# Performance work log

Measured on AMD Instinct MI355X. Metric: run time of the kernel, lower is better.

## Reference

```python
import jax, jax.numpy as jnp
import numpy as np

N_NODES = 50000
N_EDGES = 800000
IN_DIM = 1280
HID = 512
EMB = 64
LN_EPS = 1e-5
NEG_SLOPE = 0.2  # DGL GATConv default leaky_relu slope


def setup_inputs() -> dict:
    key = jax.random.key(0)
    ks = jax.random.split(key, 10)
    features = jax.random.normal(ks[0], (N_NODES, IN_DIM), dtype=jnp.float32)
    src = jax.random.randint(ks[1], (N_EDGES,), 0, N_NODES)
    dst = jax.random.randint(ks[2], (N_EDGES,), 0, N_NODES)
    # MLPBlock params: Linear(IN_DIM -> HID) + LayerNorm(HID)
    W1 = jax.random.normal(ks[3], (IN_DIM, HID), dtype=jnp.float32) / np.sqrt(IN_DIM)
    b1 = jnp.zeros((HID,), dtype=jnp.float32)
    ln_g = jnp.ones((HID,), dtype=jnp.float32)
    ln_b = jnp.zeros((HID,), dtype=jnp.float32)
    # GATConv params (num_heads=1): fc (no bias), attn_l, attn_r, output bias
    Wg = jax.random.normal(ks[4], (HID, EMB), dtype=jnp.float32) / np.sqrt(HID)
    attn_l = jax.random.normal(ks[5], (EMB,), dtype=jnp.float32) * 0.1
    attn_r = jax.random.normal(ks[6], (EMB,), dtype=jnp.float32) * 0.1
    bias_g = jnp.zeros((EMB,), dtype=jnp.float32)
    return {"features": features, "src": src, "dst": dst, "W1": W1, "b1": b1,
            "ln_g": ln_g, "ln_b": ln_b, "Wg": Wg, "attn_l": attn_l,
            "attn_r": attn_r, "bias_g": bias_g}


def reference(features, src, dst, W1, b1, ln_g, ln_b, Wg, attn_l, attn_r, bias_g):
    # MLPBlock: linear -> ReLU -> LayerNorm (dropout is identity in eval)
    x = jax.nn.relu(features @ W1 + b1)                     # [N, HID]
    mu = jnp.mean(x, axis=-1, keepdims=True)
    var = jnp.mean(jnp.square(x - mu), axis=-1, keepdims=True)
    x = (x - mu) * jax.lax.rsqrt(var + LN_EPS) * ln_g + ln_b

    # GATConv (single head)
    feat = x @ Wg                                           # [N, EMB]
    el = feat @ attn_l                                      # [N]
    er = feat @ attn_r                                      # [N]
    e = jax.nn.leaky_relu(el[src] + er[dst], NEG_SLOPE)     # [E]

    # edge softmax over incoming edges of each dst node
    m = jax.ops.segment_max(e, dst, num_segments=N_NODES)   # [N]
    ex = jnp.exp(e - m[dst])                                # [E]
    s = jax.ops.segment_sum(ex, dst, num_segments=N_NODES)  # [N]
    a = ex / s[dst]                                         # [E]

    # scatter-aggregate weighted source features
    out = jax.ops.segment_sum(a[:, None] * feat[src], dst, num_segments=N_NODES)
    return out + bias_g                                     # [N, EMB] (head dim squeezed)
```

## Files before the change

### kernel.cpp

```cpp
#include <hip/hip_runtime.h>
#include <hip/hip_bf16.h>
#include <stdint.h>

#define N_NODES 50000
#define N_EDGES 800000
#define IN_DIM 1280
#define HID 512
#define EMB 64
#define M_PAD 50048
#define MT1 391
#define LN_EPS 1e-5f

typedef __attribute__((ext_vector_type(8))) __bf16 bf16x8;
typedef __attribute__((ext_vector_type(4))) float floatx4;

#define AS1C(p) ((const __attribute__((address_space(1))) void*)(p))
#define AS3(p)  ((__attribute__((address_space(3))) void*)(p))

__device__ __forceinline__ unsigned f2bf(float f) {
  unsigned u = __float_as_uint(f);
  u += 0x7FFFu + ((u >> 16) & 1u);
  return u >> 16;
}
__device__ __forceinline__ float bf2f(unsigned short s) {
  return __uint_as_float(((unsigned)s) << 16);
}

__global__ __launch_bounds__(256) void k_prep(const float* __restrict__ W1,
                                              const float* __restrict__ Wg,
                                              const float* __restrict__ ln_g,
                                              const float* __restrict__ ln_b,
                                              unsigned short* __restrict__ B1t,
                                              unsigned short* __restrict__ Wgp,
                                              float* __restrict__ uvec,
                                              float* __restrict__ vvec,
                                              int* __restrict__ deg,
                                              float* __restrict__ s1,
                                              float* __restrict__ s2) {
  int idx = blockIdx.x * 256 + threadIdx.x;
  if (idx < HID * IN_DIM) {
    int n = idx / IN_DIM;
    int k = idx - n * IN_DIM;
    B1t[idx] = (unsigned short)f2bf(W1[(size_t)k * HID + n]);
  }
  if (idx < EMB * HID) {
    int n = idx >> 9;
    int k = idx & 511;
    Wgp[idx] = (unsigned short)f2bf(ln_g[k] * Wg[(size_t)k * EMB + n]);
  }
  if (idx < EMB) {
    float su = 0.f, sv = 0.f;
    for (int k = 0; k < HID; ++k) {
      float wv = Wg[(size_t)k * EMB + idx];
      su += ln_b[k] * wv;
      sv += ln_g[k] * wv;
    }
    uvec[idx] = su;
    vvec[idx] = sv;
  }
  if (idx < N_NODES) deg[idx] = 0;
  if (idx < M_PAD) { s1[idx] = 0.f; s2[idx] = 0.f; }
}

__global__ __launch_bounds__(256) void k_convhist(const float* __restrict__ F,
                                                  unsigned short* __restrict__ Fb,
                                                  const int* __restrict__ dst,
                                                  int* __restrict__ deg) {
  if (blockIdx.x < 31280) {
    size_t base = ((size_t)blockIdx.x * 256 + threadIdx.x) * 8;
    uint4 o;
    if (base < (size_t)N_NODES * IN_DIM) {
      float4 f0 = *(const float4*)(F + base);
      float4 f1 = *(const float4*)(F + base + 4);
      o.x = f2bf(f0.x) | (f2bf(f0.y) << 16);
      o.y = f2bf(f0.z) | (f2bf(f0.w) << 16);
      o.z = f2bf(f1.x) | (f2bf(f1.y) << 16);
      o.w = f2bf(f1.z) | (f2bf(f1.w) << 16);
    } else {
      o = make_uint4(0u, 0u, 0u, 0u);
    }
    *(uint4*)(Fb + base) = o;
  } else {
    int t = (blockIdx.x - 31280) * 256 + threadIdx.x;
    if (t < N_EDGES) atomicAdd(&deg[dst[t]], 1);
  }
}

__global__ __launch_bounds__(256) void k_gemm1(const unsigned short* __restrict__ Abf,
                                               const unsigned short* __restrict__ Bt,
                                               const float* __restrict__ bias1,
                                               unsigned short* __restrict__ xn,
                                               float* __restrict__ s1,
                                               float* __restrict__ s2) {
  __shared__ unsigned short As[128 * 64];
  __shared__ unsigned short Bs[128 * 64];
  const int t = threadIdx.x;
  const int bm = blockIdx.x, bn = blockIdx.y;
  const int w = t >> 6, lane = t & 63, quad = lane >> 4, lr = lane & 15;
  const int wm = (w & 1) * 64, wn = (w >> 1) * 64;

  floatx4 acc[4][4];
#pragma unroll
  for (int i = 0; i < 4; ++i)
#pragma unroll
    for (int j = 0; j < 4; ++j) acc[i][j] = (floatx4){0.f, 0.f, 0.f, 0.f};

  const int rr = t >> 3;
  const int cc = (t & 7) ^ (rr & 7);
  const unsigned short* aP[4];
  const unsigned short* bP[4];
#pragma unroll
  for (int j = 0; j < 4; ++j) {
    aP[j] = Abf + (size_t)(bm * 128 + j * 32 + rr) * IN_DIM + cc * 8;
    bP[j] = Bt + (size_t)(bn * 128 + j * 32 + rr) * IN_DIM + cc * 8;
  }
  unsigned short* asw = As + w * 512;
  unsigned short* bsw = Bs + w * 512;

  const int l7 = lr & 7;

  for (int k0 = 0; k0 < IN_DIM; k0 += 64) {
#pragma unroll
    for (int j = 0; j < 4; ++j) {
      __builtin_amdgcn_global_load_lds(AS1C(aP[j] + k0), AS3(asw + j * 2048), 16, 0, 0);
      __builtin_amdgcn_global_load_lds(AS1C(bP[j] + k0), AS3(bsw + j * 2048), 16, 0, 0);
    }
    __syncthreads();

#pragma unroll
    for (int h = 0; h < 2; ++h) {
      const int col = ((h * 4 + quad) ^ l7) * 8;
      bf16x8 af[4], bfv[4];
#pragma unroll
      for (int mi = 0; mi < 4; ++mi)
        af[mi] = *(const bf16x8*)&As[(wm + mi * 16 + lr) * 64 + col];
#pragma unroll
      for (int ni = 0; ni < 4; ++ni)
        bfv[ni] = *(const bf16x8*)&Bs[(wn + ni * 16 + lr) * 64 + col];
#pragma unroll
      for (int mi = 0; mi < 4; ++mi)
#pragma unroll
        for (int ni = 0; ni < 4; ++ni)
          acc[mi][ni] = __builtin_amdgcn_mfma_f32_16x16x32_bf16(af[mi], bfv[ni], acc[mi][ni], 0, 0, 0);
    }
    __syncthreads();
  }

#pragma unroll
  for (int mi = 0; mi < 4; ++mi) {
    int gr = bm * 128 + wm + mi * 16 + quad * 4;
#pragma unroll
    for (int r = 0; r < 4; ++r) {
      float ps1 = 0.f, ps2 = 0.f;
#pragma unroll
      for (int ni = 0; ni < 4; ++ni) {
        int gc = bn * 128 + wn + ni * 16 + lr;
        float v = acc[mi][ni][r] + bias1[gc];
        v = v > 0.f ? v : 0.f;
        unsigned short h = (unsigned short)f2bf(v);
        xn[(size_t)(gr + r) * HID + gc] = h;
        float vr = bf2f(h);
        ps1 += vr;
        ps2 += vr * vr;
      }
#pragma unroll
      for (int m = 1; m < 16; m <<= 1) {
        ps1 += __shfl_xor(ps1, m, 64);
        ps2 += __shfl_xor(ps2, m, 64);
      }
      if (lr == 0) {
        atomicAdd(&s1[gr + r], ps1);
        atomicAdd(&s2[gr + r], ps2);
      }
    }
  }
}

__device__ __forceinline__ int swz(int r) { return (r ^ (r >> 2)) & 3; }

__global__ __launch_bounds__(256) void k_gemm2(const unsigned short* __restrict__ Xn,
                                               const unsigned short* __restrict__ Wgp,
                                               const float* __restrict__ s1,
                                               const float* __restrict__ s2,
                                               const float* __restrict__ uvec,
                                               const float* __restrict__ vvec,
                                               const float* __restrict__ al,
                                               const float* __restrict__ ar,
                                               float* __restrict__ feat,
                                               float* __restrict__ el,
                                               float* __restrict__ er) {
  __shared__ unsigned short As[128 * 32];
  __shared__ unsigned short Bs[64 * 32];
  const int t = threadIdx.x;
  const int bm = blockIdx.x;
  const int w = t >> 6, lane = t & 63, quad = lane >> 4, lr = lane & 15;

  floatx4 acc[2][4];
#pragma unroll
  for (int i = 0; i < 2; ++i)
#pragma unroll
    for (int j = 0; j < 4; ++j) acc[i][j] = (floatx4){0.f, 0.f, 0.f, 0.f};

  const int r0 = t >> 2, c0 = (t & 3) ^ swz(t >> 2);
  const int r1 = 64 + (t >> 2), c1 = (t & 3) ^ swz(64 + (t >> 2));
  const unsigned short* a0 = Xn + (size_t)(bm * 128 + r0) * HID + c0 * 8;
  const unsigned short* a1 = Xn + (size_t)(bm * 128 + r1) * HID + c1 * 8;
  const unsigned short* b0 = Wgp + (size_t)r0 * HID + c0 * 8;
  unsigned short* asw = As + w * 512;
  unsigned short* bsw = Bs + w * 512;

  const int q2 = quad ^ swz(lr);

  for (int k0 = 0; k0 < HID; k0 += 32) {
    __builtin_amdgcn_global_load_lds(AS1C(a0 + k0), AS3(asw), 16, 0, 0);
    __builtin_amdgcn_global_load_lds(AS1C(a1 + k0), AS3(asw + 2048), 16, 0, 0);
    __builtin_amdgcn_global_load_lds(AS1C(b0 + k0), AS3(bsw), 16, 0, 0);
    __syncthreads();

    bf16x8 af[2], bfv[4];
#pragma unroll
    for (int mi = 0; mi < 2; ++mi)
      af[mi] = *(const bf16x8*)&As[(w * 32 + mi * 16 + lr) * 32 + q2 * 8];
#pragma unroll
    for (int ni = 0; ni < 4; ++ni)
      bfv[ni] = *(const bf16x8*)&Bs[(ni * 16 + lr) * 32 + q2 * 8];
#pragma unroll
    for (int mi = 0; mi < 2; ++mi)
#pragma unroll
      for (int ni = 0; ni < 4; ++ni)
        acc[mi][ni] = __builtin_amdgcn_mfma_f32_16x16x32_bf16(af[mi], bfv[ni], acc[mi][ni], 0, 0, 0);
    __syncthreads();
  }

  float alv[4], arv[4], uv[4], vv[4];
#pragma unroll
  for (int ni = 0; ni < 4; ++ni) {
    alv[ni] = al[ni * 16 + lr];
    arv[ni] = ar[ni * 16 + lr];
    uv[ni] = uvec[ni * 16 + lr];
    vv[ni] = vvec[ni * 16 + lr];
  }
#pragma unroll
  for (int mi = 0; mi < 2; ++mi) {
    int gr = bm * 128 + w * 32 + mi * 16 + quad * 4;
#pragma unroll
    for (int r = 0; r < 4; ++r) {
      int row = gr + r;
      float mu = s1[row] * (1.f / HID);
      float rs = rsqrtf(s2[row] * (1.f / HID) - mu * mu + LN_EPS);
      float mrs = mu * rs;
      float sl = 0.f, sr2 = 0.f;
#pragma unroll
      for (int ni = 0; ni < 4; ++ni) {
        float v = rs * acc[mi][ni][r] + uv[ni] - mrs * vv[ni];
        feat[(size_t)row * EMB + ni * 16 + lr] = v;
        sl += v * alv[ni];
        sr2 += v * arv[ni];
      }
#pragma unroll
      for (int m = 1; m < 16; m <<= 1) {
        sl += __shfl_xor(sl, m, 64);
        sr2 += __shfl_xor(sr2, m, 64);
      }
      if (lr == 0) {
        el[row] = sl;
        er[row] = sr2;
      }
    }
  }
}

__global__ __launch_bounds__(256) void k_scan1(const int* __restrict__ deg,
                                               int* __restrict__ rowstart,
                                               int* __restrict__ bsum) {
  __shared__ int sh[256];
  int t = threadIdx.x, i = blockIdx.x * 256 + t;
  int x = (i < N_NODES) ? deg[i] : 0;
  sh[t] = x;
  __syncthreads();
  for (int off = 1; off < 256; off <<= 1) {
    int v = (t >= off) ? sh[t - off] : 0;
    __syncthreads();
    sh[t] += v;
    __syncthreads();
  }
  if (i < N_NODES) rowstart[i] = sh[t] - x;
  if (t == 255) bsum[blockIdx.x] = sh[255];
}

__global__ __launch_bounds__(256) void k_scan23(const int* __restrict__ bsum,
                                                int* __restrict__ rowstart,
                                                int* __restrict__ cursor) {
  __shared__ int sh[256];
  int t = threadIdx.x;
  int x = (t < 196) ? bsum[t] : 0;
  sh[t] = x;
  __syncthreads();
  for (int off = 1; off < 256; off <<= 1) {
    int v = (t >= off) ? sh[t - off] : 0;
    __syncthreads();
    sh[t] += v;
    __syncthreads();
  }
  int boff = (blockIdx.x > 0) ? sh[blockIdx.x - 1] : 0;
  __syncthreads();
  int i = blockIdx.x * 256 + t;
  if (i < N_NODES) {
    int rs = rowstart[i] + boff;
    rowstart[i] = rs;
    cursor[i] = rs;
  }
}

__global__ __launch_bounds__(256) void k_fill(const int* __restrict__ src,
                                              const int* __restrict__ dst,
                                              int* __restrict__ cursor,
                                              int* __restrict__ csr_src) {
  int t = blockIdx.x * 256 + threadIdx.x;
  if (t >= N_EDGES) return;
  int pos = atomicAdd(&cursor[dst[t]], 1);
  csr_src[pos] = src[t];
}

__global__ __launch_bounds__(256) void k_gat(const int* __restrict__ rowstart,
                                             const int* __restrict__ deg,
                                             const int* __restrict__ csr_src,
                                             const float* __restrict__ el,
                                             const float* __restrict__ er,
                                             const float* __restrict__ feat,
                                             const float* __restrict__ bias_g,
                                             float* __restrict__ out) {
  int w = threadIdx.x >> 6, lane = threadIdx.x & 63;
  int v = blockIdx.x * 4 + w;
  int start = rowstart[v], d = deg[v];
  float erv = er[v];
  float s = 0.f, O = 0.f;
#pragma unroll 4
  for (int i = 0; i < d; ++i) {
    int sv = csr_src[start + i];
    float f = feat[(size_t)sv * EMB + lane];
    float e = el[sv] + erv;
    e = e > 0.f ? e : 0.2f * e;
    float p = __expf(e);
    s += p;
    O = fmaf(p, f, O);
  }
  out[(size_t)v * EMB + lane] = (d > 0 ? O / s : 0.f) + bias_g[lane];
}

extern "C" void kernel_launch(void* const* d_in, const int* in_sizes, int n_in,
                              void* d_out, int out_size, void* d_ws, size_t ws_size,
                              hipStream_t stream) {
  const float* features = (const float*)d_in[0];
  const int* src        = (const int*)d_in[1];
  const int* dst        = (const int*)d_in[2];
  const float* W1       = (const float*)d_in[3];
  const float* b1       = (const float*)d_in[4];
  const float* ln_g     = (const float*)d_in[5];
  const float* ln_b     = (const float*)d_in[6];
  const float* Wg       = (const float*)d_in[7];
  const float* attn_l   = (const float*)d_in[8];
  const float* attn_r   = (const float*)d_in[9];
  const float* bias_g   = (const float*)d_in[10];
  float* out = (float*)d_out;

  char* ws = (char*)d_ws;
  size_t off = 0;
  auto alloc = [&](size_t bytes) {
    char* p = ws + off;
    off = (off + bytes + 255) & ~(size_t)255;
    return p;
  };
  unsigned short* B1t   = (unsigned short*)alloc((size_t)HID * IN_DIM * 2);
  unsigned short* Wgp   = (unsigned short*)alloc((size_t)EMB * HID * 2);
  unsigned short* featbf= (unsigned short*)alloc((size_t)M_PAD * IN_DIM * 2);
  unsigned short* xn    = (unsigned short*)alloc((size_t)M_PAD * HID * 2);
  float* feat           = (float*)alloc((size_t)M_PAD * EMB * 4);
  float* el             = (float*)alloc((size_t)M_PAD * 4);
  float* er             = (float*)alloc((size_t)M_PAD * 4);
  float* s1             = (float*)alloc((size_t)M_PAD * 4);
  float* s2             = (float*)alloc((size_t)M_PAD * 4);
  float* uvec           = (float*)alloc(EMB * 4);
  float* vvec           = (float*)alloc(EMB * 4);
  int* deg              = (int*)alloc((size_t)N_NODES * 4);
  int* rowstart         = (int*)alloc((size_t)N_NODES * 4);
  int* cursor           = (int*)alloc((size_t)N_NODES * 4);
  int* bsum             = (int*)alloc(256 * 4);
  int* csr_src          = (int*)alloc((size_t)N_EDGES * 4);
  (void)ws_size; (void)in_sizes; (void)n_in; (void)out_size;

  k_prep<<<dim3(2560), dim3(256), 0, stream>>>(W1, Wg, ln_g, ln_b, B1t, Wgp,
                                               uvec, vvec, deg, s1, s2);
  k_convhist<<<dim3(31280 + 3125), dim3(256), 0, stream>>>(features, featbf, dst, deg);
  k_scan1<<<dim3(196), dim3(256), 0, stream>>>(deg, rowstart, bsum);
  k_scan23<<<dim3(196), dim3(256), 0, stream>>>(bsum, rowstart, cursor);
  k_fill<<<dim3(3125), dim3(256), 0, stream>>>(src, dst, cursor, csr_src);
  k_gemm1<<<dim3(MT1, 4), dim3(256), 0, stream>>>(featbf, B1t, b1, xn, s1, s2);
  k_gemm2<<<dim3(MT1), dim3(256), 0, stream>>>(xn, Wgp, s1, s2, uvec, vvec,
                                               attn_l, attn_r, feat, el, er);
  k_gat<<<dim3(12500), dim3(256), 0, stream>>>(rowstart, deg, csr_src, el, er, feat, bias_g, out);
}
```

Measured before the change: 673.4 us.

## Double-buffer LDS in both GEMMs and remap gemm1 blocks per XCD

Both GEMM kernels now keep two LDS buffers. The next K-tile is issued with global_load_lds before computing the current one, and explicit vmcnt waits plus raw s_barrier replace the two __syncthreads per iteration, so load latency overlaps MFMA work. gemm1 also moves to a 1D grid with an XCD-aware mapping that groups the four N-tiles of each M-tile onto the same XCD, aiming for better L2 reuse of the A rows. Doubling LDS per block may lower occupancy, and the hand-placed waitcnt counts must match the number of loads issued per stage.

Result: slower. 695.3 us (+3.3%).

```diff
diff --git a/kernel.cpp b/kernel.cpp
--- a/kernel.cpp
+++ b/kernel.cpp
@@ -92,10 +92,13 @@
                                                unsigned short* __restrict__ xn,
                                                float* __restrict__ s1,
                                                float* __restrict__ s2) {
-  __shared__ unsigned short As[128 * 64];
-  __shared__ unsigned short Bs[128 * 64];
+  __shared__ unsigned short As[2 * 128 * 64];
+  __shared__ unsigned short Bs[2 * 128 * 64];
   const int t = threadIdx.x;
-  const int bm = blockIdx.x, bn = blockIdx.y;
+  const int o = blockIdx.x;
+  const int xcd = o & 7, pos = o >> 3;
+  const int lin = (xcd < 4 ? xcd * 196 : 784 + (xcd - 4) * 195) + pos;
+  const int bm = lin >> 2, bn = lin & 3;
   const int w = t >> 6, lane = t & 63, quad = lane >> 4, lr = lane & 15;
   const int wm = (w & 1) * 64, wn = (w >> 1) * 64;
 
@@ -114,37 +117,53 @@
     aP[j] = Abf + (size_t)(bm * 128 + j * 32 + rr) * IN_DIM + cc * 8;
     bP[j] = Bt + (size_t)(bn * 128 + j * 32 + rr) * IN_DIM + cc * 8;
   }
-  unsigned short* asw = As + w * 512;
-  unsigned short* bsw = Bs + w * 512;
-
+  const int woff = w * 512;
   const int l7 = lr & 7;
 
-  for (int k0 = 0; k0 < IN_DIM; k0 += 64) {
-#pragma unroll
-    for (int j = 0; j < 4; ++j) {
-      __builtin_amdgcn_global_load_lds(AS1C(aP[j] + k0), AS3(asw + j * 2048), 16, 0, 0);
-      __builtin_amdgcn_global_load_lds(AS1C(bP[j] + k0), AS3(bsw + j * 2048), 16, 0, 0);
-    }
-    __syncthreads();
-
+#define STAGE1(K0, BUF) do {                                                        \
+    unsigned short* aw = As + (BUF) * 8192 + woff;                                  \
+    unsigned short* bw = Bs + (BUF) * 8192 + woff;                                  \
+    _Pragma("unroll")                                                               \
+    for (int j = 0; j < 4; ++j) {                                                   \
+      __builtin_amdgcn_global_load_lds(AS1C(aP[j] + (K0)), AS3(aw + j * 2048), 16, 0, 0); \
+      __builtin_amdgcn_global_load_lds(AS1C(bP[j] + (K0)), AS3(bw + j * 2048), 16, 0, 0); \
+    } } while (0)
+
+  STAGE1(0, 0);
+  for (int it = 0; it < 20; ++it) {
+    const int cur = it & 1;
+    if (it + 1 < 20) {
+      STAGE1((it + 1) * 64, cur ^ 1);
+      asm volatile("s_waitcnt vmcnt(8)" ::: "memory");
+    } else {
+      asm volatile("s_waitcnt vmcnt(0)" ::: "memory");
+    }
+    __builtin_amdgcn_s_barrier();
+    asm volatile("" ::: "memory");
+    __builtin_amdgcn_sched_barrier(0);
+
+    const unsigned short* Ab = As + cur * 8192;
+    const unsigned short* Bb = Bs + cur * 8192;
 #pragma unroll
     for (int h = 0; h < 2; ++h) {
       const int col = ((h * 4 + quad) ^ l7) * 8;
       bf16x8 af[4], bfv[4];
 #pragma unroll
       for (int mi = 0; mi < 4; ++mi)
-        af[mi] = *(const bf16x8*)&As[(wm + mi * 16 + lr) * 64 + col];
+        af[mi] = *(const bf16x8*)&Ab[(wm + mi * 16 + lr) * 64 + col];
 #pragma unroll
       for (int ni = 0; ni < 4; ++ni)
-        bfv[ni] = *(const bf16x8*)&Bs[(wn + ni * 16 + lr) * 64 + col];
+        bfv[ni] = *(const bf16x8*)&Bb[(wn + ni * 16 + lr) * 64 + col];
 #pragma unroll
       for (int mi = 0; mi < 4; ++mi)
 #pragma unroll
         for (int ni = 0; ni < 4; ++ni)
           acc[mi][ni] = __builtin_amdgcn_mfma_f32_16x16x32_bf16(af[mi], bfv[ni], acc[mi][ni], 0, 0, 0);
     }
-    __syncthreads();
-  }
+    asm volatile("" ::: "memory");
+    __builtin_amdgcn_s_barrier();
+  }
+#undef STAGE1
 
 #pragma unroll
   for (int mi = 0; mi < 4; ++mi) {
@@ -189,8 +208,8 @@
                                                float* __restrict__ feat,
                                                float* __restrict__ el,
                                                float* __restrict__ er) {
-  __shared__ unsigned short As[128 * 32];
-  __shared__ unsigned short Bs[64 * 32];
+  __shared__ unsigned short As[2 * 128 * 32];
+  __shared__ unsigned short Bs[2 * 64 * 32];
   const int t = threadIdx.x;
   const int bm = blockIdx.x;
   const int w = t >> 6, lane = t & 63, quad = lane >> 4, lr = lane & 15;
@@ -206,31 +225,49 @@
   const unsigned short* a0 = Xn + (size_t)(bm * 128 + r0) * HID + c0 * 8;
   const unsigned short* a1 = Xn + (size_t)(bm * 128 + r1) * HID + c1 * 8;
   const unsigned short* b0 = Wgp + (size_t)r0 * HID + c0 * 8;
-  unsigned short* asw = As + w * 512;
-  unsigned short* bsw = Bs + w * 512;
+  const int woff = w * 512;
 
   const int q2 = quad ^ swz(lr);
 
-  for (int k0 = 0; k0 < HID; k0 += 32) {
-    __builtin_amdgcn_global_load_lds(AS1C(a0 + k0), AS3(asw), 16, 0, 0);
-    __builtin_amdgcn_global_load_lds(AS1C(a1 + k0), AS3(asw + 2048), 16, 0, 0);
-    __builtin_amdgcn_global_load_lds(AS1C(b0 + k0), AS3(bsw), 16, 0, 0);
-    __syncthreads();
-
+#define STAGE2(K0, BUF) do {                                                        \
+    unsigned short* aw = As + (BUF) * 4096 + woff;                                  \
+    unsigned short* bw = Bs + (BUF) * 2048 + woff;                                  \
+    __builtin_amdgcn_global_load_lds(AS1C(a0 + (K0)), AS3(aw), 16, 0, 0);           \
+    __builtin_amdgcn_global_load_lds(AS1C(a1 + (K0)), AS3(aw + 2048), 16, 0, 0);    \
+    __builtin_amdgcn_global_load_lds(AS1C(b0 + (K0)), AS3(bw), 16, 0, 0);           \
+  } while (0)
+
+  STAGE2(0, 0);
+  for (int it = 0; it < 16; ++it) {
+    const int cur = it & 1;
+    if (it + 1 < 16) {
+      STAGE2((it + 1) * 32, cur ^ 1);
+      asm volatile("s_waitcnt vmcnt(3)" ::: "memory");
+    } else {
+      asm volatile("s_waitcnt vmcnt(0)" ::: "memory");
+    }
+    __builtin_amdgcn_s_barrier();
+    asm volatile("" ::: "memory");
+    __builtin_amdgcn_sched_barrier(0);
+
+    const unsigned short* Ab = As + cur * 4096;
+    const unsigned short* Bb = Bs + cur * 2048;
     bf16x8 af[2], bfv[4];
 #pragma unroll
     for (int mi = 0; mi < 2; ++mi)
-      af[mi] = *(const bf16x8*)&As[(w * 32 + mi * 16 + lr) * 32 + q2 * 8];
+      af[mi] = *(const bf16x8*)&Ab[(w * 32 + mi * 16 + lr) * 32 + q2 * 8];
 #pragma unroll
     for (int ni = 0; ni < 4; ++ni)
-      bfv[ni] = *(const bf16x8*)&Bs[(ni * 16 + lr) * 32 + q2 * 8];
+      bfv[ni] = *(const bf16x8*)&Bb[(ni * 16 + lr) * 32 + q2 * 8];
 #pragma unroll
     for (int mi = 0; mi < 2; ++mi)
 #pragma unroll
       for (int ni = 0; ni < 4; ++ni)
         acc[mi][ni] = __builtin_amdgcn_mfma_f32_16x16x32_bf16(af[mi], bfv[ni], acc[mi][ni], 0, 0, 0);
-    __syncthreads();
-  }
+    asm volatile("" ::: "memory");
+    __builtin_amdgcn_s_barrier();
+  }
+#undef STAGE2
 
   float alv[4], arv[4], uv[4], vv[4];
 #pragma unroll
@@ -395,7 +432,7 @@
   k_scan1<<<dim3(196), dim3(256), 0, stream>>>(deg, rowstart, bsum);
   k_scan23<<<dim3(196), dim3(256), 0, stream>>>(bsum, rowstart, cursor);
   k_fill<<<dim3(3125), dim3(256), 0, stream>>>(src, dst, cursor, csr_src);
-  k_gemm1<<<dim3(MT1, 4), dim3(256), 0, stream>>>(featbf, B1t, b1, xn, s1, s2);
+  k_gemm1<<<dim3(1564), dim3(256), 0, stream>>>(featbf, B1t, b1, xn, s1, s2);
   k_gemm2<<<dim3(MT1), dim3(256), 0, stream>>>(xn, Wgp, s1, s2, uvec, vvec,
                                                attn_l, attn_r, feat, el, er);
   k_gat<<<dim3(12500), dim3(256), 0, stream>>>(rowstart, deg, csr_src, el, er, feat, bias_g, out);
```
